# Kernel optimization log

Hardware: AMD Instinct MI355X
Metric: run time of the kernel (lower is better)

## Reference

```python
import jax, jax.numpy as jnp
import numpy as np

N_STEPS = 8  # DGL GatedGraphConv n_steps as hardcoded in GatedGCN.__init__


def _gru(a, h, Wih, Whh, bih, bhh):
    # torch.nn.GRUCell: gate order (r, z, n)
    gi = a @ Wih.T + bih          # [N, 3d]
    gh = h @ Whh.T + bhh          # [N, 3d]
    ir, iz, inn = jnp.split(gi, 3, axis=-1)
    hr, hz, hn = jnp.split(gh, 3, axis=-1)
    r = jax.nn.sigmoid(ir + hr)
    z = jax.nn.sigmoid(iz + hz)
    n = jnp.tanh(inn + r * hn)
    return (1.0 - z) * n + z * h


def _gated_conv(h, src, dst, W, b, Wih, Whh, bih, bhh):
    # DGL GatedGraphConv with a single etype: for each step,
    # message = Linear(h[src]); aggregate = sum over in-edges; h = GRU(agg, h)
    N = h.shape[0]

    def step(h, _):
        m = h @ W.T + b                                   # [N, d] linear per node (message fn)
        agg = jax.ops.segment_sum(m[src], dst, num_segments=N)  # [N, d] sum over in-edges
        return _gru(agg, h, Wih, Whh, bih, bhh), None

    h, _ = jax.lax.scan(step, h, None, length=N_STEPS)
    return h


def setup_inputs() -> dict:
    key = jax.random.key(0)
    ks = jax.random.split(key, 10)
    N, E, D = 50000, 800000, 128  # in_feats = h_feats = num_classes = 128
    s = 1.0 / np.sqrt(D)
    return {
        "in_feat": jax.random.normal(ks[0], (N, D), jnp.float32),
        "src": jax.random.randint(ks[1], (E,), 0, N),
        "dst": jax.random.randint(ks[2], (E,), 0, N),
        "W1": jax.random.normal(ks[3], (D, D), jnp.float32) * s,
        "b1": jnp.zeros((D,), jnp.float32),
        "Wih1": jax.random.normal(ks[4], (3 * D, D), jnp.float32) * s,
        "Whh1": jax.random.normal(ks[5], (3 * D, D), jnp.float32) * s,
        "bih1": jnp.zeros((3 * D,), jnp.float32),
        "bhh1": jnp.zeros((3 * D,), jnp.float32),
        "W2": jax.random.normal(ks[6], (D, D), jnp.float32) * s,
        "b2": jnp.zeros((D,), jnp.float32),
        "Wih2": jax.random.normal(ks[7], (3 * D, D), jnp.float32) * s,
        "Whh2": jax.random.normal(ks[8], (3 * D, D), jnp.float32) * s,
        "bih2": jnp.zeros((3 * D,), jnp.float32),
        "bhh2": jnp.zeros((3 * D,), jnp.float32),
    }


def reference(in_feat, src, dst, W1, b1, Wih1, Whh1, bih1, bhh1,
              W2, b2, Wih2, Whh2, bih2, bhh2):
    # in_feats == h_feats so DGL's zero-padding of the input is a no-op here.
    h = _gated_conv(in_feat, src, dst, W1, b1, Wih1, Whh1, bih1, bhh1)
    h = jax.nn.relu(h)
    h = _gated_conv(h, src, dst, W2, b2, Wih2, Whh2, bih2, bhh2)
    # dgl.mean_nodes with a single graph -> [1, num_classes]
    return jnp.mean(h, axis=0, keepdims=True)
```

## Files before the change

### kernel.cpp

```cpp
#include <hip/hip_runtime.h>
#include <hip/hip_bf16.h>
#include <cmath>

#define DD 128

typedef __attribute__((ext_vector_type(8))) short short8v;
typedef __attribute__((ext_vector_type(4))) float floatx4;

__device__ __forceinline__ float sigmoid_f(float x) { return 1.0f / (1.0f + __expf(-x)); }
__device__ __forceinline__ float tanh_f(float x) {
  float e = __expf(2.0f * x);
  return 1.0f - 2.0f / (e + 1.0f);
}
__device__ __forceinline__ unsigned short f2bf(float x) {
  __hip_bfloat16 b = __float2bfloat16(x);
  return *reinterpret_cast<unsigned short*>(&b);
}
__device__ __forceinline__ float bf2f(unsigned short s) {
  return __uint_as_float(((unsigned int)s) << 16);
}

__global__ __launch_bounds__(256) void deg_count(const int* __restrict__ dst,
                                                 int* __restrict__ deg, int E) {
  int e = blockIdx.x * blockDim.x + threadIdx.x;
  if (e < E) atomicAdd(&deg[dst[e]], 1);
}

__global__ __launch_bounds__(256) void scan_part(const int* __restrict__ deg,
                                                 int* __restrict__ bsum, int N) {
  __shared__ int s[256];
  int tid = threadIdx.x;
  int i = blockIdx.x * 256 + tid;
  s[tid] = (i < N) ? deg[i] : 0;
  __syncthreads();
  for (int st = 128; st > 0; st >>= 1) {
    if (tid < st) s[tid] += s[tid + st];
    __syncthreads();
  }
  if (tid == 0) bsum[blockIdx.x] = s[0];
}

__global__ __launch_bounds__(256) void scan_top(const int* __restrict__ bsum,
                                                int* __restrict__ bofs, int nb) {
  __shared__ int s[256];
  int tid = threadIdx.x;
  int v = (tid < nb) ? bsum[tid] : 0;
  s[tid] = v;
  __syncthreads();
  for (int o = 1; o < 256; o <<= 1) {
    int t = (tid >= o) ? s[tid - o] : 0;
    __syncthreads();
    s[tid] += t;
    __syncthreads();
  }
  if (tid < nb) bofs[tid] = s[tid] - v;
  if (tid == nb - 1) bofs[nb] = s[tid];
}

__global__ __launch_bounds__(256) void scan_final(const int* __restrict__ deg,
                                                  const int* __restrict__ bofs,
                                                  int* __restrict__ ofs,
                                                  int* __restrict__ cur, int N) {
  __shared__ int s[256];
  int tid = threadIdx.x;
  int i = blockIdx.x * 256 + tid;
  int v = (i < N) ? deg[i] : 0;
  s[tid] = v;
  __syncthreads();
  for (int o = 1; o < 256; o <<= 1) {
    int t = (tid >= o) ? s[tid - o] : 0;
    __syncthreads();
    s[tid] += t;
    __syncthreads();
  }
  int off = bofs[blockIdx.x] + s[tid] - v;
  if (i < N) {
    ofs[i] = off;
    cur[i] = off;
    if (i == N - 1) ofs[N] = off + v;
  }
}

__global__ __launch_bounds__(256) void fill_csr(const int* __restrict__ src,
                                                const int* __restrict__ dst,
                                                int* __restrict__ cur,
                                                int* __restrict__ eidx, int E) {
  int e = blockIdx.x * blockDim.x + threadIdx.x;
  if (e < E) {
    int p = atomicAdd(&cur[dst[e]], 1);
    eidx[p] = src[e];
  }
}

__global__ __launch_bounds__(128) void fuse_w(const float* __restrict__ Wih,
                                              const float* __restrict__ W,
                                              float* __restrict__ Wc32) {
  int r = blockIdx.x;
  int k = threadIdx.x;
  float acc = 0.0f;
  for (int j = 0; j < DD; ++j) acc = fmaf(Wih[r * DD + j], W[j * DD + k], acc);
  Wc32[(size_t)r * DD + k] = acc;
}

__global__ __launch_bounds__(128) void fuse_u(const float* __restrict__ Wih,
                                              const float* __restrict__ b,
                                              float* __restrict__ u) {
  int r = blockIdx.x * 128 + threadIdx.x;
  if (r < 3 * DD) {
    float acc = 0.0f;
    for (int j = 0; j < DD; ++j) acc = fmaf(Wih[r * DD + j], b[j], acc);
    u[r] = acc;
  }
}

__global__ __launch_bounds__(256) void split_w(const float* __restrict__ Wf,
                                               const float* __restrict__ Whh,
                                               unsigned short* __restrict__ Wp) {
  int i = blockIdx.x * 256 + threadIdx.x;
  const int TOT = 6 * DD * DD;
  if (i < TOT) {
    int r = i >> 7;
    float x = (r < 3 * DD) ? Wf[i] : Whh[i - 3 * DD * DD];
    unsigned short hb = f2bf(x);
    float xr = x - bf2f(hb);
    unsigned short mb = f2bf(xr);
    float x2 = xr - bf2f(mb);
    unsigned short lb = f2bf(x2);
    Wp[i] = hb;
    Wp[TOT + i] = mb;
    Wp[2 * TOT + i] = lb;
  }
}

__global__ __launch_bounds__(256) void gather_h(const float* __restrict__ h,
                                                const int* __restrict__ ofs,
                                                const int* __restrict__ eidx,
                                                float* __restrict__ agg, int N) {
  int node = blockIdx.x * 8 + (threadIdx.x >> 5);
  if (node >= N) return;
  int l = (threadIdx.x & 31) << 2;
  int beg = ofs[node], end = ofs[node + 1];
  float4 a0 = {0.f, 0.f, 0.f, 0.f}, a1 = {0.f, 0.f, 0.f, 0.f};
  float4 a2 = {0.f, 0.f, 0.f, 0.f}, a3 = {0.f, 0.f, 0.f, 0.f};
  int e = beg;
  for (; e + 3 < end; e += 4) {
    int s0 = eidx[e], s1 = eidx[e + 1], s2 = eidx[e + 2], s3 = eidx[e + 3];
    float4 v0 = *(const float4*)(h + (size_t)s0 * DD + l);
    float4 v1 = *(const float4*)(h + (size_t)s1 * DD + l);
    float4 v2 = *(const float4*)(h + (size_t)s2 * DD + l);
    float4 v3 = *(const float4*)(h + (size_t)s3 * DD + l);
    a0.x += v0.x; a0.y += v0.y; a0.z += v0.z; a0.w += v0.w;
    a1.x += v1.x; a1.y += v1.y; a1.z += v1.z; a1.w += v1.w;
    a2.x += v2.x; a2.y += v2.y; a2.z += v2.z; a2.w += v2.w;
    a3.x += v3.x; a3.y += v3.y; a3.z += v3.z; a3.w += v3.w;
  }
  for (; e + 1 < end; e += 2) {
    int s0 = eidx[e], s1 = eidx[e + 1];
    float4 v0 = *(const float4*)(h + (size_t)s0 * DD + l);
    float4 v1 = *(const float4*)(h + (size_t)s1 * DD + l);
    a0.x += v0.x; a0.y += v0.y; a0.z += v0.z; a0.w += v0.w;
    a1.x += v1.x; a1.y += v1.y; a1.z += v1.z; a1.w += v1.w;
  }
  if (e < end) {
    float4 v = *(const float4*)(h + (size_t)eidx[e] * DD + l);
    a0.x += v.x; a0.y += v.y; a0.z += v.z; a0.w += v.w;
  }
  float4 r;
  r.x = (a0.x + a1.x) + (a2.x + a3.x);
  r.y = (a0.y + a1.y) + (a2.y + a3.y);
  r.z = (a0.z + a1.z) + (a2.z + a3.z);
  r.w = (a0.w + a1.w) + (a2.w + a3.w);
  *(float4*)(agg + (size_t)node * DD + l) = r;
}

__device__ __forceinline__ void split8(const float* p, short8v& q0, short8v& q1, short8v& q2) {
  float4 v0 = *(const float4*)(p);
  float4 v1 = *(const float4*)(p + 4);
  float f[8] = {v0.x, v0.y, v0.z, v0.w, v1.x, v1.y, v1.z, v1.w};
#pragma unroll
  for (int e = 0; e < 8; ++e) {
    float x = f[e];
    unsigned short hb = f2bf(x);
    float xr = x - bf2f(hb);
    unsigned short mb = f2bf(xr);
    float x2 = xr - bf2f(mb);
    q0[e] = (short)hb;
    q1[e] = (short)mb;
    q2[e] = (short)f2bf(x2);
  }
}

__global__ __launch_bounds__(256, 2) void gru_mfma3(
    const float* __restrict__ Agg, const float* __restrict__ H,
    const unsigned short* __restrict__ Wp,
    const float* __restrict__ bih, const float* __restrict__ bhh,
    const float* __restrict__ u, const int* __restrict__ deg,
    float* __restrict__ Hout, int N, int do_relu)
{
  __shared__ short sB[2][96 * DD];
  const int TOT = 6 * DD * DD;
  const int tid = threadIdx.x;
  const int wid = tid >> 6;
  const int lane = tid & 63;
  const int lrow = lane & 15;
  const int hi = lane >> 4;
  const int lk = hi * 8;
  const int rowBase = blockIdx.x * 128 + wid * 32;
  const int j0 = blockIdx.y * 32;

  floatx4 acc[6][2][2];
#pragma unroll
  for (int g = 0; g < 6; ++g)
#pragma unroll
    for (int ct = 0; ct < 2; ++ct)
#pragma unroll
      for (int rt = 0; rt < 2; ++rt) acc[g][ct][rt] = (floatx4){0.f, 0.f, 0.f, 0.f};

  int r0 = rowBase + lrow;       if (r0 >= N) r0 = N - 1;
  int r1 = rowBase + 16 + lrow;  if (r1 >= N) r1 = N - 1;

  int s_row[6], s_cnk[6];
  size_t s_grow[6];
#pragma unroll
  for (int i = 0; i < 6; ++i) {
    int ch = tid + i * 256;
    s_row[i] = ch >> 4;
    s_cnk[i] = ch & 15;
    s_grow[i] = (size_t)((s_row[i] >> 5) * DD + j0 + (s_row[i] & 31));
  }

  short8v wreg[12];
#pragma unroll
  for (int i = 0; i < 6; ++i) {
    wreg[i]     = *(const short8v*)(Wp + 0 * TOT + s_grow[i] * DD + s_cnk[i] * 8);
    wreg[6 + i] = *(const short8v*)(Wp + 1 * TOT + s_grow[i] * DD + s_cnk[i] * 8);
  }

  short8v frag[3][4][2];
#pragma unroll
  for (int kc = 0; kc < 4; ++kc) {
    split8(Agg + (size_t)r0 * DD + kc * 32 + lk, frag[0][kc][0], frag[1][kc][0], frag[2][kc][0]);
    split8(Agg + (size_t)r1 * DD + kc * 32 + lk, frag[0][kc][1], frag[1][kc][1], frag[2][kc][1]);
  }

#pragma unroll
  for (int arr = 0; arr < 2; ++arr) {
    const size_t gbase = (size_t)arr * 384 * DD;
    if (arr > 0) __syncthreads();
#pragma unroll
    for (int i = 0; i < 6; ++i) {
      int off = s_row[i] * DD + (s_cnk[i] ^ (s_row[i] & 7)) * 8;
      *(short8v*)(&sB[0][off]) = wreg[i];
      *(short8v*)(&sB[1][off]) = wreg[6 + i];
    }
#pragma unroll
    for (int i = 0; i < 6; ++i)
      wreg[i] = *(const short8v*)(Wp + 2 * TOT + gbase + s_grow[i] * DD + s_cnk[i] * 8);
    __syncthreads();

#pragma unroll
    for (int kc = 0; kc < 4; ++kc) {
#pragma unroll
      for (int gl = 0; gl < 3; ++gl) {
#pragma unroll
        for (int ct = 0; ct < 2; ++ct) {
          int lr = gl * 32 + ct * 16 + lrow;
          int off = lr * DD + ((kc * 4 + hi) ^ (lr & 7)) * 8;
          short8v bh = *(const short8v*)(&sB[0][off]);
#pragma unroll
          for (int rt = 0; rt < 2; ++rt) {
            acc[arr * 3 + gl][ct][rt] = __builtin_amdgcn_mfma_f32_16x16x32_bf16(
                frag[0][kc][rt], bh, acc[arr * 3 + gl][ct][rt], 0, 0, 0);
            acc[arr * 3 + gl][ct][rt] = __builtin_amdgcn_mfma_f32_16x16x32_bf16(
                frag[1][kc][rt], bh, acc[arr * 3 + gl][ct][rt], 0, 0, 0);
            acc[arr * 3 + gl][ct][rt] = __builtin_amdgcn_mfma_f32_16x16x32_bf16(
                frag[2][kc][rt], bh, acc[arr * 3 + gl][ct][rt], 0, 0, 0);
          }
          short8v bm = *(const short8v*)(&sB[1][off]);
#pragma unroll
          for (int rt = 0; rt < 2; ++rt) {
            acc[arr * 3 + gl][ct][rt] = __builtin_amdgcn_mfma_f32_16x16x32_bf16(
                frag[0][kc][rt], bm, acc[arr * 3 + gl][ct][rt], 0, 0, 0);
            acc[arr * 3 + gl][ct][rt] = __builtin_amdgcn_mfma_f32_16x16x32_bf16(
                frag[1][kc][rt], bm, acc[arr * 3 + gl][ct][rt], 0, 0, 0);
          }
        }
      }
    }
    __syncthreads();

#pragma unroll
    for (int i = 0; i < 6; ++i) {
      int off = s_row[i] * DD + (s_cnk[i] ^ (s_row[i] & 7)) * 8;
      *(short8v*)(&sB[0][off]) = wreg[i];
    }
    if (arr == 0) {
      const size_t g1 = (size_t)384 * DD;
#pragma unroll
      for (int i = 0; i < 6; ++i) {
        wreg[i]     = *(const short8v*)(Wp + 0 * TOT + g1 + s_grow[i] * DD + s_cnk[i] * 8);
        wreg[6 + i] = *(const short8v*)(Wp + 1 * TOT + g1 + s_grow[i] * DD + s_cnk[i] * 8);
      }
    }
    __syncthreads();

#pragma unroll
    for (int kc = 0; kc < 4; ++kc) {
#pragma unroll
      for (int gl = 0; gl < 3; ++gl) {
#pragma unroll
        for (int ct = 0; ct < 2; ++ct) {
          int lr = gl * 32 + ct * 16 + lrow;
          int off = lr * DD + ((kc * 4 + hi) ^ (lr & 7)) * 8;
          short8v bl = *(const short8v*)(&sB[0][off]);
#pragma unroll
          for (int rt = 0; rt < 2; ++rt) {
            acc[arr * 3 + gl][ct][rt] = __builtin_amdgcn_mfma_f32_16x16x32_bf16(
                frag[0][kc][rt], bl, acc[arr * 3 + gl][ct][rt], 0, 0, 0);
          }
        }
      }
    }

    if (arr == 0) {
#pragma unroll
      for (int kc = 0; kc < 4; ++kc) {
        split8(H + (size_t)r0 * DD + kc * 32 + lk, frag[0][kc][0], frag[1][kc][0], frag[2][kc][0]);
        split8(H + (size_t)r1 * DD + kc * 32 + lk, frag[0][kc][1], frag[1][kc][1], frag[2][kc][1]);
      }
    }
  }

  float bi_r[2], bi_z[2], bi_n[2], bh_r[2], bh_z[2], bh_n[2], u_r[2], u_z[2], u_n[2];
#pragma unroll
  for (int ct = 0; ct < 2; ++ct) {
    int c = j0 + ct * 16 + lrow;
    bi_r[ct] = bih[c];  bi_z[ct] = bih[DD + c];  bi_n[ct] = bih[2 * DD + c];
    bh_r[ct] = bhh[c];  bh_z[ct] = bhh[DD + c];  bh_n[ct] = bhh[2 * DD + c];
    u_r[ct]  = u[c];    u_z[ct]  = u[DD + c];    u_n[ct]  = u[2 * DD + c];
  }

#pragma unroll
  for (int rt = 0; rt < 2; ++rt) {
#pragma unroll
    for (int q = 0; q < 4; ++q) {
      int row = rowBase + rt * 16 + hi * 4 + q;
      if (row < N) {
        float dg = (float)deg[row];
#pragma unroll
        for (int ct = 0; ct < 2; ++ct) {
          int c = j0 + ct * 16 + lrow;
          float ir = acc[0][ct][rt][q] + bi_r[ct] + dg * u_r[ct];
          float iz = acc[1][ct][rt][q] + bi_z[ct] + dg * u_z[ct];
          float in = acc[2][ct][rt][q] + bi_n[ct] + dg * u_n[ct];
          float hr = acc[3][ct][rt][q] + bh_r[ct];
          float hz = acc[4][ct][rt][q] + bh_z[ct];
          float hn = acc[5][ct][rt][q] + bh_n[ct];
          float rg = sigmoid_f(ir + hr);
          float zg = sigmoid_f(iz + hz);
          float ng = tanh_f(in + rg * hn);
          float hold = H[(size_t)row * DD + c];
          float out = (1.0f - zg) * ng + zg * hold;
          if (do_relu) out = fmaxf(out, 0.0f);
          Hout[(size_t)row * DD + c] = out;
        }
      }
    }
  }
}

__global__ __launch_bounds__(256) void col_mean(
    const float* __restrict__ H, float* __restrict__ out, int N)
{
  __shared__ float s[256];
  int c = threadIdx.x & 127;
  int rg = threadIdx.x >> 7;
  float acc = 0.0f;
  for (int r = blockIdx.x * 2 + rg; r < N; r += gridDim.x * 2)
    acc += H[(size_t)r * DD + c];
  s[threadIdx.x] = acc;
  __syncthreads();
  if (threadIdx.x < 128) {
    float v = (s[threadIdx.x] + s[threadIdx.x + 128]) * (1.0f / (float)N);
    unsafeAtomicAdd(out + c, v);
  }
}

extern "C" void kernel_launch(void* const* d_in, const int* in_sizes, int n_in,
                              void* d_out, int out_size, void* d_ws, size_t ws_size,
                              hipStream_t stream) {
  const float* in_feat = (const float*)d_in[0];
  const int* src = (const int*)d_in[1];
  const int* dst = (const int*)d_in[2];
  const float* W[2]   = {(const float*)d_in[3], (const float*)d_in[9]};
  const float* bb[2]  = {(const float*)d_in[4], (const float*)d_in[10]};
  const float* Wih[2] = {(const float*)d_in[5], (const float*)d_in[11]};
  const float* Whh[2] = {(const float*)d_in[6], (const float*)d_in[12]};
  const float* bih[2] = {(const float*)d_in[7], (const float*)d_in[13]};
  const float* bhh[2] = {(const float*)d_in[8], (const float*)d_in[14]};
  const int N = in_sizes[0] / DD;
  const int E = in_sizes[1];

  const size_t nd = (size_t)N * DD;
  char* base = (char*)d_ws;
  float* hA  = (float*)base; base += nd * sizeof(float);
  float* hB  = (float*)base; base += nd * sizeof(float);
  float* agg = (float*)base; base += nd * sizeof(float);
  float* Wc32 = (float*)base; base += (size_t)3 * DD * DD * sizeof(float);
  unsigned short* Wp[2];
  Wp[0] = (unsigned short*)base; base += (size_t)3 * 6 * DD * DD * sizeof(unsigned short);
  Wp[1] = (unsigned short*)base; base += (size_t)3 * 6 * DD * DD * sizeof(unsigned short);
  float* u[2];
  u[0] = (float*)base; base += 3 * DD * sizeof(float);
  u[1] = (float*)base; base += 3 * DD * sizeof(float);
  int* deg  = (int*)base; base += (size_t)N * sizeof(int);
  int* ofs  = (int*)base; base += ((size_t)N + 1) * sizeof(int);
  int* cur  = (int*)base; base += (size_t)N * sizeof(int);
  int* eidx = (int*)base; base += (size_t)E * sizeof(int);
  int* bsum = (int*)base; base += 256 * sizeof(int);
  int* bofs = (int*)base; base += 257 * sizeof(int);

  const int nb = (N + 255) / 256;

  hipMemsetAsync(deg, 0, (size_t)N * sizeof(int), stream);
  deg_count<<<(E + 255) / 256, 256, 0, stream>>>(dst, deg, E);
  scan_part<<<nb, 256, 0, stream>>>(deg, bsum, N);
  scan_top<<<1, 256, 0, stream>>>(bsum, bofs, nb);
  scan_final<<<nb, 256, 0, stream>>>(deg, bofs, ofs, cur, N);
  fill_csr<<<(E + 255) / 256, 256, 0, stream>>>(src, dst, cur, eidx, E);

  for (int layer = 0; layer < 2; ++layer) {
    fuse_w<<<3 * DD, 128, 0, stream>>>(Wih[layer], W[layer], Wc32);
    split_w<<<(6 * DD * DD + 255) / 256, 256, 0, stream>>>(Wc32, Whh[layer], Wp[layer]);
    fuse_u<<<3, 128, 0, stream>>>(Wih[layer], bb[layer], u[layer]);
  }

  hipMemcpyAsync(hA, in_feat, nd * sizeof(float), hipMemcpyDeviceToDevice, stream);

  float* hcur = hA;
  float* hnxt = hB;
  const int gblocks = (N + 7) / 8;
  const int mblocks = (N + 127) / 128;

  for (int layer = 0; layer < 2; ++layer) {
    for (int step_i = 0; step_i < 8; ++step_i) {
      gather_h<<<gblocks, 256, 0, stream>>>(hcur, ofs, eidx, agg, N);
      int do_relu = (layer == 0 && step_i == 7) ? 1 : 0;
      gru_mfma3<<<dim3(mblocks, 4), 256, 0, stream>>>(
          agg, hcur, Wp[layer], bih[layer], bhh[layer],
          u[layer], deg, hnxt, N, do_relu);
      float* t = hcur; hcur = hnxt; hnxt = t;
    }
  }

  hipMemsetAsync(d_out, 0, DD * sizeof(float), stream);
  col_mean<<<256, 256, 0, stream>>>(hcur, (float*)d_out, N);
}
```

Measured before the change: 2.220 ms.

## Pre-swizzle split weights into MFMA fragment order and drop LDS staging

The weight-splitting kernel now writes the three bf16 parts of each weight in a per-lane MFMA fragment layout. The GRU MFMA kernel can then load its B operands straight from global memory with one contiguous 16-byte load per lane, instead of staging them through shared memory with several __syncthreads barriers. This removes LDS traffic and block synchronisation and may allow higher occupancy. In exchange it relies on L2/L1 caching of the weights, which every row block re-reads from global memory. The gather kernel also unrolls its edge loop to 8 loads in flight to improve memory-level parallelism.

```diff
diff --git a/kernel.cpp b/kernel.cpp
--- a/kernel.cpp
+++ b/kernel.cpp
@@ -119,16 +119,34 @@
   int i = blockIdx.x * 256 + threadIdx.x;
   const int TOT = 6 * DD * DD;
   if (i < TOT) {
-    int r = i >> 7;
-    float x = (r < 3 * DD) ? Wf[i] : Whh[i - 3 * DD * DD];
+    int grow = i >> 7;
+    int k = i & 127;
+    float x = (grow < 3 * DD) ? Wf[i] : Whh[i - 3 * DD * DD];
     unsigned short hb = f2bf(x);
     float xr = x - bf2f(hb);
     unsigned short mb = f2bf(xr);
     float x2 = xr - bf2f(mb);
     unsigned short lb = f2bf(x2);
-    Wp[i] = hb;
-    Wp[TOT + i] = mb;
-    Wp[2 * TOT + i] = lb;
+
+    int arr = grow >> 8 >> 1;
+    arr = (grow >= 384) ? 1 : 0;
+    int g2 = grow - arr * 384;
+    int gl = g2 >> 7;
+    int colg = g2 & 127;
+    int jb = colg >> 5;
+    int cc = colg & 31;
+    int ct = cc >> 4;
+    int lrow = cc & 15;
+    int kc = k >> 5;
+    int k2 = k & 31;
+    int hi = k2 >> 3;
+    int e = k2 & 7;
+    int lane = hi * 16 + lrow;
+    int tileBase = ((((jb * 2 + arr) * 4 + kc) * 3 + gl) * 2 + ct) * 3;
+    size_t off = (size_t)tileBase * 512 + lane * 8 + e;
+    Wp[off] = hb;
+    Wp[off + 512] = mb;
+    Wp[off + 1024] = lb;
   }
 }
 
@@ -140,36 +158,36 @@
   if (node >= N) return;
   int l = (threadIdx.x & 31) << 2;
   int beg = ofs[node], end = ofs[node + 1];
-  float4 a0 = {0.f, 0.f, 0.f, 0.f}, a1 = {0.f, 0.f, 0.f, 0.f};
-  float4 a2 = {0.f, 0.f, 0.f, 0.f}, a3 = {0.f, 0.f, 0.f, 0.f};
+  float4 aa[4];
+#pragma unroll
+  for (int j = 0; j < 4; ++j) aa[j] = (float4){0.f, 0.f, 0.f, 0.f};
   int e = beg;
-  for (; e + 3 < end; e += 4) {
-    int s0 = eidx[e], s1 = eidx[e + 1], s2 = eidx[e + 2], s3 = eidx[e + 3];
-    float4 v0 = *(const float4*)(h + (size_t)s0 * DD + l);
-    float4 v1 = *(const float4*)(h + (size_t)s1 * DD + l);
-    float4 v2 = *(const float4*)(h + (size_t)s2 * DD + l);
-    float4 v3 = *(const float4*)(h + (size_t)s3 * DD + l);
-    a0.x += v0.x; a0.y += v0.y; a0.z += v0.z; a0.w += v0.w;
-    a1.x += v1.x; a1.y += v1.y; a1.z += v1.z; a1.w += v1.w;
-    a2.x += v2.x; a2.y += v2.y; a2.z += v2.z; a2.w += v2.w;
-    a3.x += v3.x; a3.y += v3.y; a3.z += v3.z; a3.w += v3.w;
+  for (; e + 7 < end; e += 8) {
+    float4 v[8];
+#pragma unroll
+    for (int j = 0; j < 8; ++j)
+      v[j] = *(const float4*)(h + (size_t)eidx[e + j] * DD + l);
+#pragma unroll
+    for (int j = 0; j < 8; ++j) {
+      aa[j & 3].x += v[j].x; aa[j & 3].y += v[j].y;
+      aa[j & 3].z += v[j].z; aa[j & 3].w += v[j].w;
+    }
   }
   for (; e + 1 < end; e += 2) {
-    int s0 = eidx[e], s1 = eidx[e + 1];
-    float4 v0 = *(const float4*)(h + (size_t)s0 * DD + l);
-    float4 v1 = *(const float4*)(h + (size_t)s1 * DD + l);
-    a0.x += v0.x; a0.y += v0.y; a0.z += v0.z; a0.w += v0.w;
-    a1.x += v1.x; a1.y += v1.y; a1.z += v1.z; a1.w += v1.w;
+    float4 v0 = *(const float4*)(h + (size_t)eidx[e] * DD + l);
+    float4 v1 = *(const float4*)(h + (size_t)eidx[e + 1] * DD + l);
+    aa[0].x += v0.x; aa[0].y += v0.y; aa[0].z += v0.z; aa[0].w += v0.w;
+    aa[1].x += v1.x; aa[1].y += v1.y; aa[1].z += v1.z; aa[1].w += v1.w;
   }
   if (e < end) {
     float4 v = *(const float4*)(h + (size_t)eidx[e] * DD + l);
-    a0.x += v.x; a0.y += v.y; a0.z += v.z; a0.w += v.w;
+    aa[0].x += v.x; aa[0].y += v.y; aa[0].z += v.z; aa[0].w += v.w;
   }
   float4 r;
-  r.x = (a0.x + a1.x) + (a2.x + a3.x);
-  r.y = (a0.y + a1.y) + (a2.y + a3.y);
-  r.z = (a0.z + a1.z) + (a2.z + a3.z);
-  r.w = (a0.w + a1.w) + (a2.w + a3.w);
+  r.x = (aa[0].x + aa[1].x) + (aa[2].x + aa[3].x);
+  r.y = (aa[0].y + aa[1].y) + (aa[2].y + aa[3].y);
+  r.z = (aa[0].z + aa[1].z) + (aa[2].z + aa[3].z);
+  r.w = (aa[0].w + aa[1].w) + (aa[2].w + aa[3].w);
   *(float4*)(agg + (size_t)node * DD + l) = r;
 }
 
@@ -197,8 +215,6 @@
     const float* __restrict__ u, const int* __restrict__ deg,
     float* __restrict__ Hout, int N, int do_relu)
 {
-  __shared__ short sB[2][96 * DD];
-  const int TOT = 6 * DD * DD;
   const int tid = threadIdx.x;
   const int wid = tid >> 6;
   const int lane = tid & 63;
@@ -206,7 +222,8 @@
   const int hi = lane >> 4;
   const int lk = hi * 8;
   const int rowBase = blockIdx.x * 128 + wid * 32;
-  const int j0 = blockIdx.y * 32;
+  const int jb = blockIdx.y;
+  const int j0 = jb * 32;
 
   floatx4 acc[6][2][2];
 #pragma unroll
@@ -219,114 +236,38 @@
   int r0 = rowBase + lrow;       if (r0 >= N) r0 = N - 1;
   int r1 = rowBase + 16 + lrow;  if (r1 >= N) r1 = N - 1;
 
-  int s_row[6], s_cnk[6];
-  size_t s_grow[6];
-#pragma unroll
-  for (int i = 0; i < 6; ++i) {
-    int ch = tid + i * 256;
-    s_row[i] = ch >> 4;
-    s_cnk[i] = ch & 15;
-    s_grow[i] = (size_t)((s_row[i] >> 5) * DD + j0 + (s_row[i] & 31));
-  }
-
-  short8v wreg[12];
-#pragma unroll
-  for (int i = 0; i < 6; ++i) {
-    wreg[i]     = *(const short8v*)(Wp + 0 * TOT + s_grow[i] * DD + s_cnk[i] * 8);
-    wreg[6 + i] = *(const short8v*)(Wp + 1 * TOT + s_grow[i] * DD + s_cnk[i] * 8);
-  }
-
   short8v frag[3][4][2];
-#pragma unroll
-  for (int kc = 0; kc < 4; ++kc) {
-    split8(Agg + (size_t)r0 * DD + kc * 32 + lk, frag[0][kc][0], frag[1][kc][0], frag[2][kc][0]);
-    split8(Agg + (size_t)r1 * DD + kc * 32 + lk, frag[0][kc][1], frag[1][kc][1], frag[2][kc][1]);
-  }
 
 #pragma unroll
   for (int arr = 0; arr < 2; ++arr) {
-    const size_t gbase = (size_t)arr * 384 * DD;
-    if (arr > 0) __syncthreads();
-#pragma unroll
-    for (int i = 0; i < 6; ++i) {
-      int off = s_row[i] * DD + (s_cnk[i] ^ (s_row[i] & 7)) * 8;
-      *(short8v*)(&sB[0][off]) = wreg[i];
-      *(short8v*)(&sB[1][off]) = wreg[6 + i];
-    }
-#pragma unroll
-    for (int i = 0; i < 6; ++i)
-      wreg[i] = *(const short8v*)(Wp + 2 * TOT + gbase + s_grow[i] * DD + s_cnk[i] * 8);
-    __syncthreads();
-
+    const float* A = arr ? H : Agg;
 #pragma unroll
     for (int kc = 0; kc < 4; ++kc) {
+      split8(A + (size_t)r0 * DD + kc * 32 + lk, frag[0][kc][0], frag[1][kc][0], frag[2][kc][0]);
+      split8(A + (size_t)r1 * DD + kc * 32 + lk, frag[0][kc][1], frag[1][kc][1], frag[2][kc][1]);
+    }
+    const unsigned short* wbase = Wp + (size_t)(jb * 2 + arr) * 36864 + lane * 8;
+#pragma unroll
+    for (int kc = 0; kc < 4; ++kc) {
 #pragma unroll
       for (int gl = 0; gl < 3; ++gl) {
 #pragma unroll
         for (int ct = 0; ct < 2; ++ct) {
-          int lr = gl * 32 + ct * 16 + lrow;
-          int off = lr * DD + ((kc * 4 + hi) ^ (lr & 7)) * 8;
-          short8v bh = *(const short8v*)(&sB[0][off]);
+          const unsigned short* t = wbase + kc * 9216 + gl * 3072 + ct * 1536;
+          short8v b0 = *(const short8v*)(t);
+          short8v b1 = *(const short8v*)(t + 512);
+          short8v b2 = *(const short8v*)(t + 1024);
+          const int g = arr * 3 + gl;
 #pragma unroll
           for (int rt = 0; rt < 2; ++rt) {
-            acc[arr * 3 + gl][ct][rt] = __builtin_amdgcn_mfma_f32_16x16x32_bf16(
-                frag[0][kc][rt], bh, acc[arr * 3 + gl][ct][rt], 0, 0, 0);
-            acc[arr * 3 + gl][ct][rt] = __builtin_amdgcn_mfma_f32_16x16x32_bf16(
-                frag[1][kc][rt], bh, acc[arr * 3 + gl][ct][rt], 0, 0, 0);
-            acc[arr * 3 + gl][ct][rt] = __builtin_amdgcn_mfma_f32_16x16x32_bf16(
-                frag[2][kc][rt], bh, acc[arr * 3 + gl][ct][rt], 0, 0, 0);
-          }
-          short8v bm = *(const short8v*)(&sB[1][off]);
-#pragma unroll
-          for (int rt = 0; rt < 2; ++rt) {
-            acc[arr * 3 + gl][ct][rt] = __builtin_amdgcn_mfma_f32_16x16x32_bf16(
-                frag[0][kc][rt], bm, acc[arr * 3 + gl][ct][rt], 0, 0, 0);
-            acc[arr * 3 + gl][ct][rt] = __builtin_amdgcn_mfma_f32_16x16x32_bf16(
-                frag[1][kc][rt], bm, acc[arr * 3 + gl][ct][rt], 0, 0, 0);
+            acc[g][ct][rt] = __builtin_amdgcn_mfma_f32_16x16x32_bf16(frag[0][kc][rt], b0, acc[g][ct][rt], 0, 0, 0);
+            acc[g][ct][rt] = __builtin_amdgcn_mfma_f32_16x16x32_bf16(frag[1][kc][rt], b0, acc[g][ct][rt], 0, 0, 0);
+            acc[g][ct][rt] = __builtin_amdgcn_mfma_f32_16x16x32_bf16(frag[2][kc][rt], b0, acc[g][ct][rt], 0, 0, 0);
+            acc[g][ct][rt] = __builtin_amdgcn_mfma_f32_16x16x32_bf16(frag[0][kc][rt], b1, acc[g][ct][rt], 0, 0, 0);
+            acc[g][ct][rt] = __builtin_amdgcn_mfma_f32_16x16x32_bf16(frag[1][kc][rt], b1, acc[g][ct][rt], 0, 0, 0);
+            acc[g][ct][rt] = __builtin_amdgcn_mfma_f32_16x16x32_bf16(frag[0][kc][rt], b2, acc[g][ct][rt], 0, 0, 0);
           }
         }
-      }
-    }
-    __syncthreads();
-
-#pragma unroll
-    for (int i = 0; i < 6; ++i) {
-      int off = s_row[i] * DD + (s_cnk[i] ^ (s_row[i] & 7)) * 8;
-      *(short8v*)(&sB[0][off]) = wreg[i];
-    }
-    if (arr == 0) {
-      const size_t g1 = (size_t)384 * DD;
-#pragma unroll
-      for (int i = 0; i < 6; ++i) {
-        wreg[i]     = *(const short8v*)(Wp + 0 * TOT + g1 + s_grow[i] * DD + s_cnk[i] * 8);
-        wreg[6 + i] = *(const short8v*)(Wp + 1 * TOT + g1 + s_grow[i] * DD + s_cnk[i] * 8);
-      }
-    }
-    __syncthreads();
-
-#pragma unroll
-    for (int kc = 0; kc < 4; ++kc) {
-#pragma unroll
-      for (int gl = 0; gl < 3; ++gl) {
-#pragma unroll
-        for (int ct = 0; ct < 2; ++ct) {
-          int lr = gl * 32 + ct * 16 + lrow;
-          int off = lr * DD + ((kc * 4 + hi) ^ (lr & 7)) * 8;
-          short8v bl = *(const short8v*)(&sB[0][off]);
-#pragma unroll
-          for (int rt = 0; rt < 2; ++rt) {
-            acc[arr * 3 + gl][ct][rt] = __builtin_amdgcn_mfma_f32_16x16x32_bf16(
-                frag[0][kc][rt], bl, acc[arr * 3 + gl][ct][rt], 0, 0, 0);
-          }
-        }
-      }
-    }
-
-    if (arr == 0) {
-#pragma unroll
-      for (int kc = 0; kc < 4; ++kc) {
-        split8(H + (size_t)r0 * DD + kc * 32 + lk, frag[0][kc][0], frag[1][kc][0], frag[2][kc][0]);
-        split8(H + (size_t)r1 * DD + kc * 32 + lk, frag[0][kc][1], frag[1][kc][1], frag[2][kc][1]);
       }
     }
   }
```

Result: slower. 2.987 ms (+34.6%).
